# Kernel optimization log

Hardware: AMD Instinct MI355X
Metric: run time of the kernel (lower is better)

## Reference

```python
import jax, jax.numpy as jnp
import numpy as np


def setup_inputs() -> dict:
    key = jax.random.key(0)
    ks = jax.random.split(key, 8)
    B, C, H, W = 8, 512, 64, 64
    Co = C // 8
    s = 0.02  # weight init scale
    return {
        'x': jax.random.normal(ks[0], (B, C, H, W), jnp.float32),
        'Wq': jax.random.normal(ks[1], (Co, C), jnp.float32) * s,
        'bq': jnp.zeros((Co,), jnp.float32),
        'Wk': jax.random.normal(ks[2], (Co, C), jnp.float32) * s,
        'bk': jnp.zeros((Co,), jnp.float32),
        'Wv': jax.random.normal(ks[3], (C, C), jnp.float32) * s,
        'bv': jnp.zeros((C,), jnp.float32),
        'gamma': jax.random.normal(ks[4], (1,), jnp.float32) * 0.1,
    }


def reference(x, Wq, bq, Wk, bk, Wv, bv, gamma):
    B, C, H, W = x.shape
    # 1x1 convs == channel contractions
    q = jnp.einsum('oc,bchw->bohw', Wq, x) + bq[None, :, None, None]
    k = jnp.einsum('oc,bchw->bohw', Wk, x) + bk[None, :, None, None]
    v = jnp.einsum('oc,bchw->bohw', Wv, x) + bv[None, :, None, None]
    # column (H-axis) energies, diagonal masked to -inf to avoid double count
    eH = jnp.einsum('bohw,boiw->bhwi', q, k)  # [B,H,W,H2]
    diag_mask = jnp.where(jnp.eye(H, dtype=bool), -jnp.inf, 0.0)  # [H,H2]
    eH = eH + diag_mask[None, :, None, :]
    # row (W-axis) energies
    eW = jnp.einsum('bohw,bohj->bhwj', q, k)  # [B,H,W,W2]
    # joint softmax over concatenated H+W axis
    attn = jax.nn.softmax(jnp.concatenate([eH, eW], axis=-1), axis=-1)
    aH, aW = attn[..., :H], attn[..., H:]
    out = jnp.einsum('bciw,bhwi->bchw', v, aH) + jnp.einsum('bchj,bhwj->bchw', v, aW)
    return gamma[0] * out + x
```

## Files before the change

kernel.cpp:

```cpp
#include <hip/hip_runtime.h>
#include <hip/hip_bf16.h>

#define NB 8
#define NC 512
#define NO 64
#define NH 64
#define NW 64
#define NHW 4096

typedef __attribute__((ext_vector_type(8))) short bf16x8;
typedef __attribute__((ext_vector_type(4))) float f32x4;

__device__ __forceinline__ void gload16(const void* g, void* l) {
    __builtin_amdgcn_global_load_lds(
        (const __attribute__((address_space(1))) void*)g,
        (__attribute__((address_space(3))) void*)l, 16, 0, 0);
}

__device__ __forceinline__ short f2bf_bits(float f) {
    __hip_bfloat16 h = __float2bfloat16(f);
    short s; __builtin_memcpy(&s, &h, 2); return s;
}
__device__ __forceinline__ float bfbits_to_f(short s) {
    unsigned int u = ((unsigned int)(unsigned short)s) << 16;
    float f; __builtin_memcpy(&f, &u, 4); return f;
}

__global__ __launch_bounds__(256) void pack_w(
    const float* __restrict__ Wq, const float* __restrict__ bq,
    const float* __restrict__ Wk, const float* __restrict__ bk,
    const float* __restrict__ Wv, const float* __restrict__ bv,
    __hip_bfloat16* __restrict__ Wbf, float* __restrict__ bias_all)
{
    const int row = blockIdx.x;
    const int t = threadIdx.x;
    const float* src; float bias;
    if (row < 64)       { src = Wq + row*NC;        bias = bq[row]; }
    else if (row < 128) { src = Wk + (row-64)*NC;   bias = bk[row-64]; }
    else                { src = Wv + (row-128)*NC;  bias = bv[row-128]; }
    for (int i = t; i < NC; i += 256)
        Wbf[(size_t)row*NC + i] = __float2bfloat16(src[i]);
    if (t == 0) bias_all[row] = bias;
}

__global__ __launch_bounds__(256) void qkv_fused(
    const float* __restrict__ x, const __hip_bfloat16* __restrict__ Wbf,
    const float* __restrict__ bias_all,
    __hip_bfloat16* __restrict__ qkT2, __hip_bfloat16* __restrict__ vb)
{
    __shared__ __align__(16) char As[2][16384];
    __shared__ __align__(16) char Bs[2][16384];
    const int t = threadIdx.x;
    const int lane = t & 63;
    const int wv = t >> 6;
    const int wm = wv >> 1, wn = wv & 1;
    const int fr = lane & 15, fg = lane >> 4;
    const int hw0 = blockIdx.x * 128;
    const int y   = blockIdx.y;
    const int b   = blockIdx.z;
    const int o0s = (y == 4) ? 0 : (128 + y*128);
    const float* xb = x + (size_t)b*NC*NHW + hw0;
    const int oct = t >> 5, hwg = t & 31;

    float4 xr[8];

#define STAGE_A(ksrc, buf)                                                  \
    {                                                                       \
        _Pragma("unroll")                                                   \
        for (int s = 0; s < 4; ++s) {                                       \
            int linear = s*256 + t;                                         \
            int row = linear >> 3, g = linear & 7;                          \
            int gk = (g ^ (row & 7)) * 8;                                   \
            gload16(Wbf + (size_t)(o0s + row)*NC + (ksrc)*64 + gk,          \
                    As[buf] + linear*16);                                   \
        }                                                                   \
    }
#define LOAD_B(ksrc)                                                        \
    {                                                                       \
        const float* gp = xb + (size_t)((ksrc)*64 + oct*8)*NHW + hwg*4;     \
        _Pragma("unroll")                                                   \
        for (int e = 0; e < 8; ++e)                                         \
            xr[e] = *(const float4*)(gp + (size_t)e*NHW);                   \
    }
#define WRITE_B(buf)                                                        \
    {                                                                       \
        _Pragma("unroll")                                                   \
        for (int d = 0; d < 4; ++d) {                                       \
            int row = hwg*4 + d;                                            \
            bf16x8 wv8;                                                     \
            _Pragma("unroll")                                               \
            for (int e = 0; e < 8; ++e)                                     \
                wv8[e] = f2bf_bits(((const float*)&xr[e])[d]);              \
            int slot = oct ^ (row & 7) ^ ((row >> 3) & 7);                  \
            *(bf16x8*)(Bs[buf] + row*128 + (slot << 4)) = wv8;              \
        }                                                                   \
    }
#define BSLOT(c, gl) (((gl) ^ ((c) & 7) ^ (((c) >> 3) & 7)) << 4)

    LOAD_B(0);
    STAGE_A(0, 0);
    WRITE_B(0);
    __syncthreads();

    f32x4 acc[4][4] = {};

    for (int ks = 0; ks < 8; ++ks) {
        const int cur = ks & 1, nxt = cur ^ 1;
        if (ks < 7) { LOAD_B(ks+1); STAGE_A(ks+1, nxt); }
        #pragma unroll
        for (int kk = 0; kk < 2; ++kk) {
            const int gl = kk*4 + fg;
            bf16x8 m1[4], n1[4];
            if (y == 4) {
                #pragma unroll
                for (int mf = 0; mf < 4; ++mf) {
                    int r = wm*64 + mf*16 + fr;
                    m1[mf] = *(const bf16x8*)(Bs[cur] + r*128 + BSLOT(r, gl));
                }
                #pragma unroll
                for (int nf = 0; nf < 4; ++nf) {
                    int c = wn*64 + nf*16 + fr;
                    n1[nf] = *(const bf16x8*)(As[cur] + c*128 + ((gl ^ (c & 7)) << 4));
                }
            } else {
                #pragma unroll
                for (int mf = 0; mf < 4; ++mf) {
                    int r = wm*64 + mf*16 + fr;
                    m1[mf] = *(const bf16x8*)(As[cur] + r*128 + ((gl ^ (r & 7)) << 4));
                }
                #pragma unroll
                for (int nf = 0; nf < 4; ++nf) {
                    int c = wn*64 + nf*16 + fr;
                    n1[nf] = *(const bf16x8*)(Bs[cur] + c*128 + BSLOT(c, gl));
                }
            }
            #pragma unroll
            for (int mf = 0; mf < 4; ++mf)
                #pragma unroll
                for (int nf = 0; nf < 4; ++nf)
                    acc[mf][nf] = __builtin_amdgcn_mfma_f32_16x16x32_bf16(
                        m1[mf], n1[nf], acc[mf][nf], 0, 0, 0);
        }
        if (ks < 7) {
            WRITE_B(nxt);
            __syncthreads();
        }
    }
#undef STAGE_A
#undef LOAD_B
#undef WRITE_B
#undef BSLOT

    if (y < 4) {
        #pragma unroll
        for (int mf = 0; mf < 4; ++mf) {
            #pragma unroll
            for (int reg = 0; reg < 4; ++reg) {
                int o = o0s + wm*64 + mf*16 + (lane >> 4)*4 + reg;
                float bias = bias_all[o];
                size_t rowbase = ((size_t)b*NC + (o - 128))*NHW;
                #pragma unroll
                for (int nf = 0; nf < 4; ++nf) {
                    int hw = hw0 + wn*64 + nf*16 + (lane & 15);
                    vb[rowbase + hw] = __float2bfloat16(acc[mf][nf][reg] + bias);
                }
            }
        }
    } else {
        #pragma unroll
        for (int mf = 0; mf < 4; ++mf) {
            #pragma unroll
            for (int reg = 0; reg < 4; ++reg) {
                int hwl = wm*64 + mf*16 + (lane >> 4)*4 + reg;
                size_t rbase = ((size_t)b*NHW + hw0 + hwl)*128;
                #pragma unroll
                for (int nf = 0; nf < 4; ++nf) {
                    int col = wn*64 + nf*16 + (lane & 15);
                    qkT2[rbase + col] = __float2bfloat16(acc[mf][nf][reg] + bias_all[col]);
                }
            }
        }
    }
}

__global__ __launch_bounds__(256) void transpose_hw(
    const __hip_bfloat16* __restrict__ src_, __hip_bfloat16* __restrict__ dst_,
    int nch)
{
    __shared__ __align__(16) short tile[4][64*64];
    const int t = threadIdx.x, wv = t >> 6, lane = t & 63;
    const int c = blockIdx.x*4 + wv, b = blockIdx.y;
    const __hip_bfloat16* src = src_ + ((size_t)(b*nch + c))*NHW;
    __hip_bfloat16* dst = dst_ + ((size_t)(b*nch + c))*NHW;
    short* tl = tile[wv];
    #pragma unroll
    for (int s = 0; s < 8; ++s) {
        int i = s*8 + (lane>>3), w0 = (lane&7)*8;
        bf16x8 vv = *(const bf16x8*)(src + i*64 + w0);
        *(bf16x8*)&tl[i*64 + (((w0>>3) ^ ((i>>3)&7)) << 3)] = vv;
    }
    __syncthreads();
    #pragma unroll
    for (int s = 0; s < 8; ++s) {
        int w = s*8 + (lane>>3), i0 = (lane&7)*8;
        bf16x8 ov;
        #pragma unroll
        for (int d = 0; d < 8; ++d)
            ov[d] = tl[(i0+d)*64 + (((w>>3) ^ (lane&7)) << 3) + (w&7)];
        *(bf16x8*)(dst + w*64 + i0) = ov;
    }
}

__global__ __launch_bounds__(256) void scores_mfma(
    const __hip_bfloat16* __restrict__ qkT2,
    __hip_bfloat16* __restrict__ rawH, __hip_bfloat16* __restrict__ rawW)
{
    __shared__ __align__(16) char Qs[64*128];
    __shared__ __align__(16) char Ks[64*128];
    const int t = threadIdx.x, lane = t & 63, wv = t >> 6;
    const int wm = wv >> 1, wn = wv & 1;
    const int fr = lane & 15, fg = lane >> 4;
    const int s = blockIdx.x, y = blockIdx.y, b = blockIdx.z;
    const __hip_bfloat16* base = qkT2 + (size_t)b * NHW * 128;
    #pragma unroll
    for (int i = 0; i < 2; ++i) {
        int linear = i*256 + t;
        int r = linear >> 3, g = linear & 7;
        int gk = (g ^ (r & 7)) * 8;
        size_t ro = (y == 0) ? ((size_t)(r*64 + s) * 128)
                             : ((size_t)(s*64 + r) * 128);
        gload16(base + ro + gk,      Qs + linear*16);
        gload16(base + ro + 64 + gk, Ks + linear*16);
    }
    __syncthreads();
    f32x4 acc[2][2] = {};
    #pragma unroll
    for (int kk = 0; kk < 2; ++kk) {
        const int gl = kk*4 + fg;
        bf16x8 qf[2], kf[2];
        #pragma unroll
        for (int mf = 0; mf < 2; ++mf) {
            int r = wm*32 + mf*16 + fr;
            qf[mf] = *(const bf16x8*)(Qs + r*128 + ((gl ^ (r & 7)) << 4));
        }
        #pragma unroll
        for (int nf = 0; nf < 2; ++nf) {
            int c = wn*32 + nf*16 + fr;
            kf[nf] = *(const bf16x8*)(Ks + c*128 + ((gl ^ (c & 7)) << 4));
        }
        #pragma unroll
        for (int mf = 0; mf < 2; ++mf)
            #pragma unroll
            for (int nf = 0; nf < 2; ++nf)
                acc[mf][nf] = __builtin_amdgcn_mfma_f32_16x16x32_bf16(
                    qf[mf], kf[nf], acc[mf][nf], 0, 0, 0);
    }
    __hip_bfloat16* dst = (y == 0) ? rawH : rawW;
    const size_t dbase = ((size_t)(b*64 + s)) * 4096;
    #pragma unroll
    for (int mf = 0; mf < 2; ++mf) {
        #pragma unroll
        for (int reg = 0; reg < 4; ++reg) {
            int row = wm*32 + mf*16 + (lane >> 4)*4 + reg;
            #pragma unroll
            for (int nf = 0; nf < 2; ++nf) {
                int col = wn*32 + nf*16 + (lane & 15);
                dst[dbase + (size_t)row*64 + col] = __float2bfloat16(acc[mf][nf][reg]);
            }
        }
    }
}

__global__ __launch_bounds__(256) void softmax_ab(
    const __hip_bfloat16* __restrict__ rawH, const __hip_bfloat16* __restrict__ rawW,
    __hip_bfloat16* __restrict__ aHb, __hip_bfloat16* __restrict__ aWb)
{
    __shared__ float sH[64][65];
    __shared__ float sW[64][65];
    __shared__ float red[8][64];
    const int t = threadIdx.x;
    const int w = t & 63, p = t >> 6;
    const int hb = blockIdx.x, b = blockIdx.y;
    #pragma unroll
    for (int i2 = 0; i2 < 2; ++i2) {
        int linear = i2*256 + t;
        int ww = linear >> 3, g = linear & 7;
        bf16x8 hv = *(const bf16x8*)(rawH + (((size_t)(b*64 + ww))*64 + hb)*64 + g*8);
        bf16x8 wvv = *(const bf16x8*)(rawW + (((size_t)(b*64 + hb))*64 + ww)*64 + g*8);
        #pragma unroll
        for (int e = 0; e < 8; ++e) {
            sH[ww][g*8+e] = bfbits_to_f(hv[e]);
            sW[ww][g*8+e] = bfbits_to_f(wvv[e]);
        }
    }
    __syncthreads();
    if (t < 64) sH[t][hb] = -1e30f;
    __syncthreads();
    float m = -1e30f;
    #pragma unroll
    for (int z = 0; z < 32; ++z) {
        float val = (p < 2) ? sH[w][p*32+z] : sW[w][(p-2)*32+z];
        m = fmaxf(m, val);
    }
    red[p][w] = m;
    __syncthreads();
    float M = fmaxf(fmaxf(red[0][w], red[1][w]), fmaxf(red[2][w], red[3][w]));
    float ssum = 0.f;
    #pragma unroll
    for (int z = 0; z < 32; ++z) {
        float* slot = (p < 2) ? &sH[w][p*32+z] : &sW[w][(p-2)*32+z];
        float e = __expf(*slot - M);
        ssum += e;
        *slot = e;
    }
    red[4+p][w] = ssum;
    __syncthreads();
    float S = red[4][w] + red[5][w] + red[6][w] + red[7][w];
    float rinv = 1.f / S;
    if (p < 2) {
        size_t base = (((size_t)b*NH + w)*NH + hb)*NO + p*32;
        #pragma unroll
        for (int zz = 0; zz < 4; ++zz) {
            bf16x8 pk;
            #pragma unroll
            for (int d = 0; d < 8; ++d)
                pk[d] = f2bf_bits(sH[w][p*32 + zz*8 + d] * rinv);
            *(bf16x8*)(aHb + base + zz*8) = pk;
        }
    } else {
        size_t base = (((size_t)b*NH + hb)*NH + w)*NO + (p-2)*32;
        #pragma unroll
        for (int zz = 0; zz < 4; ++zz) {
            bf16x8 pk;
            #pragma unroll
            for (int d = 0; d < 8; ++d)
                pk[d] = f2bf_bits(sW[w][(p-2)*32 + zz*8 + d] * rinv);
            *(bf16x8*)(aWb + base + zz*8) = pk;
        }
    }
}

__global__ __launch_bounds__(256) void col_mfma(
    const __hip_bfloat16* __restrict__ vT, const __hip_bfloat16* __restrict__ aH,
    __hip_bfloat16* __restrict__ PT)
{
    __shared__ __align__(16) char As[64*128];
    __shared__ __align__(16) char Bs[256*128];
    const int t = threadIdx.x, lane = t & 63, wn = t >> 6;
    const int fr = lane & 15, fg = lane >> 4;
    const int w = blockIdx.x, chalf = blockIdx.y, b = blockIdx.z;
    const __hip_bfloat16* Ag = aH + ((size_t)(b*NH + w))*4096;
    const __hip_bfloat16* Bg = vT + ((size_t)(b*NC + chalf*256))*NHW + w*64;
    #pragma unroll
    for (int s = 0; s < 2; ++s) {
        int linear = s*256 + t;
        int r = linear >> 3, g = linear & 7;
        gload16(Ag + r*64 + ((g ^ (r&7)) * 8), As + linear*16);
    }
    #pragma unroll
    for (int s = 0; s < 8; ++s) {
        int linear = s*256 + t;
        int r = linear >> 3, g = linear & 7;
        gload16(Bg + (size_t)r*NHW + ((g ^ (r&7)) * 8), Bs + linear*16);
    }
    __syncthreads();
    f32x4 acc[4][4] = {};
    #pragma unroll
    for (int kk = 0; kk < 2; ++kk) {
        int gl = kk*4 + fg;
        bf16x8 af[4], bfv[4];
        #pragma unroll
        for (int mf = 0; mf < 4; ++mf) {
            int r = mf*16 + fr;
            af[mf] = *(const bf16x8*)(As + r*128 + ((gl ^ (r&7)) << 4));
        }
        #pragma unroll
        for (int nf = 0; nf < 4; ++nf) {
            int c = wn*64 + nf*16 + fr;
            bfv[nf] = *(const bf16x8*)(Bs + c*128 + ((gl ^ (c&7)) << 4));
        }
        #pragma unroll
        for (int mf = 0; mf < 4; ++mf)
            #pragma unroll
            for (int nf = 0; nf < 4; ++nf)
                acc[mf][nf] = __builtin_amdgcn_mfma_f32_16x16x32_bf16(
                    af[mf], bfv[nf], acc[mf][nf], 0, 0, 0);
    }
    const size_t base = ((size_t)(b*NH + w))*64*512 + chalf*256;
    #pragma unroll
    for (int mf = 0; mf < 4; ++mf) {
        #pragma unroll
        for (int reg = 0; reg < 4; ++reg) {
            int hh = mf*16 + (lane >> 4)*4 + reg;
            #pragma unroll
            for (int nf = 0; nf < 4; ++nf) {
                int cc = wn*64 + nf*16 + (lane & 15);
                PT[base + (size_t)hh*512 + cc] = __float2bfloat16(acc[mf][nf][reg]);
            }
        }
    }
}

__global__ __launch_bounds__(256) void row_mfma(
    const __hip_bfloat16* __restrict__ vb, const __hip_bfloat16* __restrict__ aW,
    const __hip_bfloat16* __restrict__ PT, const float* __restrict__ x,
    const float* __restrict__ gamma, float* __restrict__ out)
{
    __shared__ __align__(16) char Ws[64*128];
    __shared__ __align__(16) char Vs[128*128];
    __shared__ __align__(16) short PTs[64*136];
    const int t = threadIdx.x, lane = t & 63, wm = t >> 6;
    const int fr = lane & 15, fg = lane >> 4;
    const int h = blockIdx.x, cq = blockIdx.y, b = blockIdx.z;
    const int c0 = cq*128;
    const __hip_bfloat16* Ag = aW + ((size_t)(b*NH + h))*4096;
    const __hip_bfloat16* Vg = vb + ((size_t)(b*NC + c0))*NHW + h*64;
    #pragma unroll
    for (int s = 0; s < 2; ++s) {
        int linear = s*256 + t;
        int r = linear >> 3, g = linear & 7;
        gload16(Ag + r*64 + ((g ^ (r&7)) * 8), Ws + linear*16);
    }
    #pragma unroll
    for (int s = 0; s < 4; ++s) {
        int linear = s*256 + t;
        int r = linear >> 3, g = linear & 7;
        gload16(Vg + (size_t)r*NHW + ((g ^ (r&7)) * 8), Vs + linear*16);
    }
    #pragma unroll
    for (int s = 0; s < 4; ++s) {
        int idx = s*256 + t;
        int ww = idx >> 4, cg = idx & 15;
        bf16x8 pv = *(const bf16x8*)(PT + (((size_t)(b*NH + ww))*64 + h)*512 + c0 + cg*8);
        *(bf16x8*)&PTs[ww*136 + cg*8] = pv;
    }
    __syncthreads();
    f32x4 acc[2][4] = {};
    #pragma unroll
    for (int kk = 0; kk < 2; ++kk) {
        int gl = kk*4 + fg;
        bf16x8 vf[2], wf[4];
        #pragma unroll
        for (int mf = 0; mf < 2; ++mf) {
            int c = wm*32 + mf*16 + fr;
            vf[mf] = *(const bf16x8*)(Vs + c*128 + ((gl ^ (c&7)) << 4));
        }
        #pragma unroll
        for (int nf = 0; nf < 4; ++nf) {
            int ww = nf*16 + fr;
            wf[nf] = *(const bf16x8*)(Ws + ww*128 + ((gl ^ (ww&7)) << 4));
        }
        #pragma unroll
        for (int mf = 0; mf < 2; ++mf)
            #pragma unroll
            for (int nf = 0; nf < 4; ++nf)
                acc[mf][nf] = __builtin_amdgcn_mfma_f32_16x16x32_bf16(
                    vf[mf], wf[nf], acc[mf][nf], 0, 0, 0);
    }
    const float g = gamma[0];
    #pragma unroll
    for (int mf = 0; mf < 2; ++mf) {
        #pragma unroll
        for (int reg = 0; reg < 4; ++reg) {
            int cl = wm*32 + mf*16 + (lane >> 4)*4 + reg;
            size_t rowbase = ((size_t)(b*NC + c0 + cl)*NH + h)*NW;
            #pragma unroll
            for (int nf = 0; nf < 4; ++nf) {
                int ww = nf*16 + (lane & 15);
                float ptv = bfbits_to_f(PTs[ww*136 + cl]);
                out[rowbase + ww] = g*(acc[mf][nf][reg] + ptv) + x[rowbase + ww];
            }
        }
    }
}

extern "C" void kernel_launch(void* const* d_in, const int* in_sizes, int n_in,
                              void* d_out, int out_size, void* d_ws, size_t ws_size,
                              hipStream_t stream) {
    (void)in_sizes; (void)n_in; (void)out_size; (void)ws_size;
    const float* x     = (const float*)d_in[0];
    const float* Wq    = (const float*)d_in[1];
    const float* bq    = (const float*)d_in[2];
    const float* Wk    = (const float*)d_in[3];
    const float* bk    = (const float*)d_in[4];
    const float* Wv    = (const float*)d_in[5];
    const float* bv    = (const float*)d_in[6];
    const float* gamma = (const float*)d_in[7];
    float* out = (float*)d_out;

    char* p = (char*)d_ws;
    __hip_bfloat16* Wbf  = (__hip_bfloat16*)(p);
    float* bias_all      = (float*)(p + 655360);
    __hip_bfloat16* qkT2 = (__hip_bfloat16*)(p + 657920);
    __hip_bfloat16* vb   = (__hip_bfloat16*)(p + 9046528);
    __hip_bfloat16* vT   = (__hip_bfloat16*)(p + 42600960);
    __hip_bfloat16* aHb  = (__hip_bfloat16*)(p + 76155392);
    __hip_bfloat16* aWb  = (__hip_bfloat16*)(p + 80349696);
    __hip_bfloat16* PT   = (__hip_bfloat16*)(p + 84544000);
    __hip_bfloat16* rawH = PT;
    __hip_bfloat16* rawW = (__hip_bfloat16*)(p + 84544000 + 8388608);

    pack_w<<<dim3(640), 256, 0, stream>>>(Wq, bq, Wk, bk, Wv, bv, Wbf, bias_all);
    qkv_fused<<<dim3(32, 5, NB), 256, 0, stream>>>(x, Wbf, bias_all, qkT2, vb);
    transpose_hw<<<dim3(128, NB), 256, 0, stream>>>(vb, vT, NC);
    scores_mfma<<<dim3(64, 2, NB), 256, 0, stream>>>(qkT2, rawH, rawW);
    softmax_ab<<<dim3(NH, NB), 256, 0, stream>>>(rawH, rawW, aHb, aWb);
    col_mfma<<<dim3(NW, 2, NB), 256, 0, stream>>>(vT, aHb, PT);
    row_mfma<<<dim3(NH, 4, NB), 256, 0, stream>>>(vb, aWb, PT, x, gamma, out);
}
```

Measured before the change: 117.7 us.

## Read QKV weights directly from global memory and deepen x prefetch to two stages

The weight tile is no longer staged through LDS; each wave loads its MFMA weight fragments straight from global memory, which are reused across blocks and likely cache-resident. The x tile is now prefetched two k-steps ahead using two register buffers, and the k-loop is fully unrolled. This halves LDS use and removes the async LDS copy, but adds many uncoalesced global loads in the inner loop and raises register pressure, which may hurt occupancy.

```diff
diff --git a/kernel.cpp b/kernel.cpp
--- a/kernel.cpp
+++ b/kernel.cpp
@@ -48,7 +48,6 @@
     const float* __restrict__ bias_all,
     __hip_bfloat16* __restrict__ qkT2, __hip_bfloat16* __restrict__ vb)
 {
-    __shared__ __align__(16) char As[2][16384];
     __shared__ __align__(16) char Bs[2][16384];
     const int t = threadIdx.x;
     const int lane = t & 63;
@@ -61,52 +60,43 @@
     const int o0s = (y == 4) ? 0 : (128 + y*128);
     const float* xb = x + (size_t)b*NC*NHW + hw0;
     const int oct = t >> 5, hwg = t & 31;
-
-    float4 xr[8];
-
-#define STAGE_A(ksrc, buf)                                                  \
-    {                                                                       \
-        _Pragma("unroll")                                                   \
-        for (int s = 0; s < 4; ++s) {                                       \
-            int linear = s*256 + t;                                         \
-            int row = linear >> 3, g = linear & 7;                          \
-            int gk = (g ^ (row & 7)) * 8;                                   \
-            gload16(Wbf + (size_t)(o0s + row)*NC + (ksrc)*64 + gk,          \
-                    As[buf] + linear*16);                                   \
-        }                                                                   \
-    }
-#define LOAD_B(ksrc)                                                        \
-    {                                                                       \
-        const float* gp = xb + (size_t)((ksrc)*64 + oct*8)*NHW + hwg*4;     \
+    const __hip_bfloat16* Wrow = Wbf + (size_t)o0s*NC;
+
+    float4 xrA[8], xrB[8];
+
+#define LOADB(j, XR) do {                                                   \
+        const float* gp = xb + (size_t)((j)*64 + oct*8)*NHW + hwg*4;        \
         _Pragma("unroll")                                                   \
         for (int e = 0; e < 8; ++e)                                         \
-            xr[e] = *(const float4*)(gp + (size_t)e*NHW);                   \
-    }
-#define WRITE_B(buf)                                                        \
-    {                                                                       \
+            XR[e] = *(const float4*)(gp + (size_t)e*NHW);                   \
+    } while (0)
+#define WRITEB(XR, buf) do {                                                \
         _Pragma("unroll")                                                   \
         for (int d = 0; d < 4; ++d) {                                       \
             int row = hwg*4 + d;                                            \
             bf16x8 wv8;                                                     \
             _Pragma("unroll")                                               \
             for (int e = 0; e < 8; ++e)                                     \
-                wv8[e] = f2bf_bits(((const float*)&xr[e])[d]);              \
+                wv8[e] = f2bf_bits(((const float*)&XR[e])[d]);              \
             int slot = oct ^ (row & 7) ^ ((row >> 3) & 7);                  \
             *(bf16x8*)(Bs[buf] + row*128 + (slot << 4)) = wv8;              \
         }                                                                   \
-    }
+    } while (0)
 #define BSLOT(c, gl) (((gl) ^ ((c) & 7) ^ (((c) >> 3) & 7)) << 4)
 
-    LOAD_B(0);
-    STAGE_A(0, 0);
-    WRITE_B(0);
+    LOADB(0, xrA);
+    LOADB(1, xrB);
+    WRITEB(xrA, 0);
     __syncthreads();
 
     f32x4 acc[4][4] = {};
 
+    #pragma unroll
     for (int ks = 0; ks < 8; ++ks) {
-        const int cur = ks & 1, nxt = cur ^ 1;
-        if (ks < 7) { LOAD_B(ks+1); STAGE_A(ks+1, nxt); }
+        const int cur = ks & 1;
+        if (ks < 6) {
+            if ((ks & 1) == 0) { LOADB(ks+2, xrA); } else { LOADB(ks+2, xrB); }
+        }
         #pragma unroll
         for (int kk = 0; kk < 2; ++kk) {
             const int gl = kk*4 + fg;
@@ -120,13 +110,13 @@
                 #pragma unroll
                 for (int nf = 0; nf < 4; ++nf) {
                     int c = wn*64 + nf*16 + fr;
-                    n1[nf] = *(const bf16x8*)(As[cur] + c*128 + ((gl ^ (c & 7)) << 4));
+                    n1[nf] = *(const bf16x8*)(Wrow + (size_t)c*NC + ks*64 + gl*8);
                 }
             } else {
                 #pragma unroll
                 for (int mf = 0; mf < 4; ++mf) {
                     int r = wm*64 + mf*16 + fr;
-                    m1[mf] = *(const bf16x8*)(As[cur] + r*128 + ((gl ^ (r & 7)) << 4));
+                    m1[mf] = *(const bf16x8*)(Wrow + (size_t)r*NC + ks*64 + gl*8);
                 }
                 #pragma unroll
                 for (int nf = 0; nf < 4; ++nf) {
@@ -142,13 +132,12 @@
                         m1[mf], n1[nf], acc[mf][nf], 0, 0, 0);
         }
         if (ks < 7) {
-            WRITE_B(nxt);
+            if (ks & 1) { WRITEB(xrA, (ks+1)&1); } else { WRITEB(xrB, (ks+1)&1); }
             __syncthreads();
         }
     }
-#undef STAGE_A
-#undef LOAD_B
-#undef WRITE_B
+#undef LOADB
+#undef WRITEB
 #undef BSLOT
 
     if (y < 4) {
```

Result: slower. 137.3 us (+16.7%).
